# Kernel optimization log

Measured on AMD Instinct MI355X. Metric: run time of the kernel, lower is better.

Reference implementation:

```python
import jax, jax.numpy as jnp
import numpy as np

_T_DURATION = 0.2
_C = 0.206756


def setup_inputs() -> dict:
    key = jax.random.key(0)
    k1, k2, k3, k4 = jax.random.split(key, 4)
    B, Nt = 512, 32768
    # normalised params (unused by the analytic path, kept for signature fidelity)
    h = jax.random.normal(k1, (B, 3), dtype=jnp.float32)
    # uniform time grid over the PFWD pulse duration [0, 0.2] s
    t = jnp.linspace(0.0, _T_DURATION, Nt, dtype=jnp.float32)
    # pressure history ~ typical PFWD peak 150 kPa, non-negative half-sine-ish pulse
    u = jax.random.uniform(k2, (B, Nt), dtype=jnp.float32)
    pulse = jnp.sin(jnp.pi * t / _T_DURATION)[None, :]  # (1, Nt) in [0,1]
    p = 150000.0 * pulse * (0.8 + 0.4 * u)  # Pa, peak ~150 kPa
    # physical params inside documented ranges: E1 [1e8,2e9], E2 [1e7,2e8], eta [1e4,5e6]
    r = jax.random.uniform(k3, (B, 3), dtype=jnp.float32)
    lo = jnp.array([1.0e8, 1.0e7, 1.0e4], dtype=jnp.float32)
    hi = jnp.array([2.0e9, 2.0e8, 5.0e6], dtype=jnp.float32)
    h_raw = lo + r * (hi - lo)
    return {"h": h, "t": t, "p": p, "h_raw": h_raw}


def reference(h, t, p, h_raw):
    """omega_i = sum_{j<=i} g(t_i - t_j) * dp_j,
    g(tau) = C*[1/(E1+E2) + E1/(E2*(E1+E2))*(1 - exp(-alpha*tau))],
    alpha  = E1*E2 / ((E1+E2)*eta).
    Exact O(Nt) reformulation: g = (A+D) - D*exp(-alpha*tau) with
    A = C/(E1+E2), D = C*E1/(E2*(E1+E2)), so
    omega_i = (A+D)*p_i - D*s_i,  s_i = exp(-alpha*dt_i)*s_{i-1} + dp_i.
    """
    E1, E2, eta = h_raw[:, 0], h_raw[:, 1], h_raw[:, 2]  # (B,)
    alpha = E1 * E2 / ((E1 + E2) * eta)                   # (B,)
    A = _C / (E1 + E2)                                    # (B,)
    D = _C * E1 / (E2 * (E1 + E2))                        # (B,)
    dp = jnp.diff(p, axis=1, prepend=0.0)                 # (B, Nt), dp_0 = p_0
    dt = jnp.diff(t, prepend=t[0])                        # (Nt,),  dt_0 = 0
    decay = jnp.exp(-alpha[:, None] * dt[None, :])        # (B, Nt)

    def step(s, xs):
        d, dpi = xs                                       # each (B,)
        s = d * s + dpi
        return s, s

    s0 = jnp.zeros(p.shape[0], dtype=p.dtype)
    _, s = jax.lax.scan(step, s0, (decay.T, dp.T))        # s: (Nt, B)
    s = s.T                                               # (B, Nt)
    omega = (A + D)[:, None] * p - D[:, None] * s         # (B, Nt), metres
    return omega
```

## Files before the change

### kernel.cpp

```cpp
#include <hip/hip_runtime.h>

#define TPB 512
#define ROUNDS 16
#define WAVE 64
#define NW (TPB / WAVE)

__global__ __launch_bounds__(TPB, 4)
void fused_scan(const float* __restrict__ tt, const float* __restrict__ p,
                const float* __restrict__ h_raw, float* __restrict__ out, int Nt)
{
    const int row  = blockIdx.x;
    const int t    = threadIdx.x;
    const int lane = t & (WAVE - 1);
    const int wid  = t >> 6;

    const float E1  = h_raw[row * 3 + 0];
    const float E2  = h_raw[row * 3 + 1];
    const float eta = h_raw[row * 3 + 2];
    const float alpha = (E1 * E2) / ((E1 + E2) * eta);
    const float A = 0.206756f / (E1 + E2);
    const float D = 0.206756f * E1 / (E2 * (E1 + E2));
    const float dtm = (tt[Nt - 1] - tt[0]) / (float)(Nt - 1);
    const float omd = -expm1f(-alpha * dtm);
    const float d   = 1.0f - omd;
    const float K1  = (A + D) - D / d;
    const float K2  = D * omd / d;

    const float d4 = (d * d) * (d * d);
    float d4l = 1.0f;
    {
        float b = d4;
        #pragma unroll
        for (int i = 0; i < 6; ++i) { if (lane & (1 << i)) d4l *= b; b *= b; }
    }

    const long long base = (long long)row * (long long)Nt;
    const float4* pg = reinterpret_cast<const float4*>(p + base);
    float4*       og = reinterpret_cast<float4*>(out + base);

    float4 v[ROUNDS];
    #pragma unroll
    for (int r = 0; r < ROUNDS; ++r) v[r] = pg[r * TPB + t];

    float x[ROUNDS];
    #pragma unroll
    for (int r = 0; r < ROUNDS; ++r)
        x[r] = fmaf(fmaf(fmaf(v[r].x, d, v[r].y), d, v[r].z), d, v[r].w);

    float m = d4;
    #pragma unroll
    for (int k = 1; k < WAVE; k <<= 1) {
        #pragma unroll
        for (int r = 0; r < ROUNDS; ++r) {
            const float y = __shfl_up(x[r], k);
            if (lane >= k) x[r] = fmaf(m, y, x[r]);
        }
        m *= m;
    }
    const float d256 = m;
    float d256w = 1.0f;
    {
        float b = d256;
        #pragma unroll
        for (int i = 0; i < 3; ++i) { if (wid & (1 << i)) d256w *= b; b *= b; }
    }
    float d2048 = d256;
    d2048 *= d2048; d2048 *= d2048; d2048 *= d2048;

    __shared__ float sw[ROUNDS][NW];
    if (lane == WAVE - 1) {
        #pragma unroll
        for (int r = 0; r < ROUNDS; ++r) sw[r][wid] = x[r];
    }
    __syncthreads();

    float C = 0.0f;
    #pragma unroll
    for (int r = 0; r < ROUNDS; ++r) {
        const float4 sA = *reinterpret_cast<const float4*>(&sw[r][0]);
        const float4 sB = *reinterpret_cast<const float4*>(&sw[r][4]);
        float run = 0.0f, E = 0.0f;
        #define STEP(w, val) { if (wid == (w)) E = run; run = fmaf(d256, run, (val)); }
        STEP(0, sA.x) STEP(1, sA.y) STEP(2, sA.z) STEP(3, sA.w)
        STEP(4, sB.x) STEP(5, sB.y) STEP(6, sB.z) STEP(7, sB.w)
        #undef STEP
        const float Bt = run;

        float wexcl = __shfl_up(x[r], 1);
        if (lane == 0) wexcl = 0.0f;

        const float seed = fmaf(fmaf(C, d256w, E), d4l, wexcl);

        const float4 pv = v[r];
        float W = seed;
        float4 o;
        W = fmaf(W, d, pv.x); o.x = fmaf(K2, W, K1 * pv.x);
        W = fmaf(W, d, pv.y); o.y = fmaf(K2, W, K1 * pv.y);
        W = fmaf(W, d, pv.z); o.z = fmaf(K2, W, K1 * pv.z);
        W = fmaf(W, d, pv.w); o.w = fmaf(K2, W, K1 * pv.w);
        og[r * TPB + t] = o;

        C = fmaf(d2048, C, Bt);
    }
}

extern "C" void kernel_launch(void* const* d_in, const int* in_sizes, int n_in,
                              void* d_out, int out_size, void* d_ws, size_t ws_size,
                              hipStream_t stream)
{
    const float* tt    = (const float*)d_in[1];
    const float* p     = (const float*)d_in[2];
    const float* h_raw = (const float*)d_in[3];
    float* out = (float*)d_out;

    const int Nt = in_sizes[1];
    const int B  = in_sizes[2] / Nt;
    if (Nt != ROUNDS * TPB * 4) return;

    fused_scan<<<B, TPB, 0, stream>>>(tt, p, h_raw, out, Nt);
}
```

Before: 24.75 us.

## Split block scan into four chunks with double-buffered shared totals

The 16 rounds of intra-wave scan, cross-wave combine and store are split into four chunks of four rounds, each with its own barrier and a double-buffered shared array of wave totals. Stores of early chunks can start while later chunks are still scanning, and fewer scan values are live at once, which lowers register pressure. The cost is four barriers instead of one. The power constants are now computed directly up front rather than as by-products of the scan loop.

After: 24.22 us, median of 2. -2.1%, faster.

```diff
diff --git a/kernel.cpp b/kernel.cpp
--- a/kernel.cpp
+++ b/kernel.cpp
@@ -2,6 +2,8 @@
 
 #define TPB 512
 #define ROUNDS 16
+#define NCHUNK 4
+#define RPC (ROUNDS / NCHUNK)
 #define WAVE 64
 #define NW (TPB / WAVE)
 
@@ -27,11 +29,22 @@
     const float K2  = D * omd / d;
 
     const float d4 = (d * d) * (d * d);
+    float d256 = d4;
+    #pragma unroll
+    for (int i = 0; i < 6; ++i) d256 *= d256;
+    float d2048 = d256;
+    d2048 *= d2048; d2048 *= d2048; d2048 *= d2048;
     float d4l = 1.0f;
     {
         float b = d4;
         #pragma unroll
         for (int i = 0; i < 6; ++i) { if (lane & (1 << i)) d4l *= b; b *= b; }
+    }
+    float d256w = 1.0f;
+    {
+        float b = d256;
+        #pragma unroll
+        for (int i = 0; i < 3; ++i) { if (wid & (1 << i)) d256w *= b; b *= b; }
     }
 
     const long long base = (long long)row * (long long)Nt;
@@ -42,65 +55,65 @@
     #pragma unroll
     for (int r = 0; r < ROUNDS; ++r) v[r] = pg[r * TPB + t];
 
-    float x[ROUNDS];
-    #pragma unroll
-    for (int r = 0; r < ROUNDS; ++r)
-        x[r] = fmaf(fmaf(fmaf(v[r].x, d, v[r].y), d, v[r].z), d, v[r].w);
-
-    float m = d4;
-    #pragma unroll
-    for (int k = 1; k < WAVE; k <<= 1) {
-        #pragma unroll
-        for (int r = 0; r < ROUNDS; ++r) {
-            const float y = __shfl_up(x[r], k);
-            if (lane >= k) x[r] = fmaf(m, y, x[r]);
-        }
-        m *= m;
-    }
-    const float d256 = m;
-    float d256w = 1.0f;
-    {
-        float b = d256;
-        #pragma unroll
-        for (int i = 0; i < 3; ++i) { if (wid & (1 << i)) d256w *= b; b *= b; }
-    }
-    float d2048 = d256;
-    d2048 *= d2048; d2048 *= d2048; d2048 *= d2048;
-
-    __shared__ float sw[ROUNDS][NW];
-    if (lane == WAVE - 1) {
-        #pragma unroll
-        for (int r = 0; r < ROUNDS; ++r) sw[r][wid] = x[r];
-    }
-    __syncthreads();
+    __shared__ float sw[2][RPC][NW];
 
     float C = 0.0f;
+
     #pragma unroll
-    for (int r = 0; r < ROUNDS; ++r) {
-        const float4 sA = *reinterpret_cast<const float4*>(&sw[r][0]);
-        const float4 sB = *reinterpret_cast<const float4*>(&sw[r][4]);
-        float run = 0.0f, E = 0.0f;
-        #define STEP(w, val) { if (wid == (w)) E = run; run = fmaf(d256, run, (val)); }
-        STEP(0, sA.x) STEP(1, sA.y) STEP(2, sA.z) STEP(3, sA.w)
-        STEP(4, sB.x) STEP(5, sB.y) STEP(6, sB.z) STEP(7, sB.w)
-        #undef STEP
-        const float Bt = run;
+    for (int c = 0; c < NCHUNK; ++c) {
+        float x[RPC], wex[RPC];
+        #pragma unroll
+        for (int j = 0; j < RPC; ++j) {
+            const float4 pv = v[c * RPC + j];
+            x[j] = fmaf(fmaf(fmaf(pv.x, d, pv.y), d, pv.z), d, pv.w);
+        }
 
-        float wexcl = __shfl_up(x[r], 1);
-        if (lane == 0) wexcl = 0.0f;
+        float m = d4;
+        #pragma unroll
+        for (int k = 1; k < WAVE; k <<= 1) {
+            #pragma unroll
+            for (int j = 0; j < RPC; ++j) {
+                const float y = __shfl_up(x[j], k);
+                if (lane >= k) x[j] = fmaf(m, y, x[j]);
+            }
+            m *= m;
+        }
+        #pragma unroll
+        for (int j = 0; j < RPC; ++j) {
+            wex[j] = __shfl_up(x[j], 1);
+            if (lane == 0) wex[j] = 0.0f;
+        }
 
-        const float seed = fmaf(fmaf(C, d256w, E), d4l, wexcl);
+        if (lane == WAVE - 1) {
+            #pragma unroll
+            for (int j = 0; j < RPC; ++j) sw[c & 1][j][wid] = x[j];
+        }
+        __syncthreads();
 
-        const float4 pv = v[r];
-        float W = seed;
-        float4 o;
-        W = fmaf(W, d, pv.x); o.x = fmaf(K2, W, K1 * pv.x);
-        W = fmaf(W, d, pv.y); o.y = fmaf(K2, W, K1 * pv.y);
-        W = fmaf(W, d, pv.z); o.z = fmaf(K2, W, K1 * pv.z);
-        W = fmaf(W, d, pv.w); o.w = fmaf(K2, W, K1 * pv.w);
-        og[r * TPB + t] = o;
+        #pragma unroll
+        for (int j = 0; j < RPC; ++j) {
+            const float4 sA = *reinterpret_cast<const float4*>(&sw[c & 1][j][0]);
+            const float4 sB = *reinterpret_cast<const float4*>(&sw[c & 1][j][4]);
+            float run = 0.0f, E = 0.0f;
+            #define STEP(w, val) { if (wid == (w)) E = run; run = fmaf(d256, run, (val)); }
+            STEP(0, sA.x) STEP(1, sA.y) STEP(2, sA.z) STEP(3, sA.w)
+            STEP(4, sB.x) STEP(5, sB.y) STEP(6, sB.z) STEP(7, sB.w)
+            #undef STEP
+            const float Bt = run;
 
-        C = fmaf(d2048, C, Bt);
+            const float seed = fmaf(fmaf(C, d256w, E), d4l, wex[j]);
+
+            const float4 pv = v[c * RPC + j];
+            float W = seed;
+            float4 o;
+            W = fmaf(W, d, pv.x); o.x = fmaf(K2, W, K1 * pv.x);
+            W = fmaf(W, d, pv.y); o.y = fmaf(K2, W, K1 * pv.y);
+            W = fmaf(W, d, pv.z); o.z = fmaf(K2, W, K1 * pv.z);
+            W = fmaf(W, d, pv.w); o.w = fmaf(K2, W, K1 * pv.w);
+            og[(c * RPC + j) * TPB + t] = o;
+
+            C = fmaf(d2048, C, Bt);
+        }
     }
 }
 
```
